# Optimization experiments

Hardware: AMD Instinct MI355X
Metric: run time of the kernel (lower is better)

## Reference

```python
import jax, jax.numpy as jnp
import numpy as np

BSZ, L, D_INNER, D_STATE = 2, 2048, 2048, 8
DT_RANK = D_INNER // 8  # 256


def setup_inputs() -> dict:
    key = jax.random.key(0)
    k0, k1, k2, k3 = jax.random.split(key, 4)
    x = jax.random.normal(k0, (BSZ, L, D_INNER), jnp.float32)
    # x_proj: Linear(d_inner -> dt_rank + 2*d_state), no bias
    W_xproj = jax.random.normal(k1, (DT_RANK + 2 * D_STATE, D_INNER), jnp.float32) * 0.02
    # dt_proj: Linear(dt_rank -> d_inner), uniform(-dt_rank^-0.5, +)
    std = DT_RANK ** -0.5
    W_dt = jax.random.uniform(k2, (D_INNER, DT_RANK), jnp.float32, -std, std)
    # dt bias init: inverse-softplus of dt ~ LogUniform(1e-3, 1e-1)
    dt = jnp.exp(jax.random.uniform(k3, (D_INNER,), jnp.float32)
                 * (jnp.log(0.1) - jnp.log(0.001)) + jnp.log(0.001))
    dt = jnp.clip(dt, 1e-4)
    b_dt = dt + jnp.log(-jnp.expm1(-dt))
    # A = repeat(arange(1, N+1), 'n -> d n'); A_log = log(A)
    A_log = jnp.log(jnp.broadcast_to(
        jnp.arange(1, D_STATE + 1, dtype=jnp.float32), (D_INNER, D_STATE)))
    D_param = jnp.ones((D_INNER,), jnp.float32)
    return {"x": x, "W_xproj": W_xproj, "W_dt": W_dt, "b_dt": b_dt,
            "A_log": A_log, "D_param": D_param}


def reference(x, W_xproj, W_dt, b_dt, A_log, D_param):
    # x: (B, L, D)
    d_state = A_log.shape[1]
    dt_rank = W_dt.shape[1]
    x_dbl = jnp.einsum('bld,kd->blk', x, W_xproj)          # (B,L,dt_rank+2N)
    dt_r = x_dbl[..., :dt_rank]
    B_ssm = x_dbl[..., dt_rank:dt_rank + d_state]          # (B,L,N)
    C_ssm = x_dbl[..., dt_rank + d_state:]                 # (B,L,N)
    delta = jax.nn.softplus(jnp.einsum('blr,dr->bld', dt_r, W_dt) + b_dt)  # (B,L,D) > 0
    A = -jnp.exp(A_log)                                     # (D,N) < 0
    # Discretization: dA = exp(delta*A), dBu = delta*B*u
    dA = jnp.exp(delta[..., None] * A)                      # (B,L,D,N)
    dBu = (delta * x)[..., None] * B_ssm[:, :, None, :]     # (B,L,D,N)

    # Linear recurrence h_t = dA_t * h_{t-1} + dBu_t via associative scan over L
    def combine(c1, c2):
        a1, b1 = c1
        a2, b2 = c2
        return a1 * a2, a2 * b1 + b2

    _, h = jax.lax.associative_scan(combine, (dA, dBu), axis=1)  # (B,L,D,N)
    y = jnp.einsum('bldn,bln->bld', h, C_ssm) + x * D_param
    return y
```

## Files before the change

### kernel.cpp

```cpp
#include <hip/hip_runtime.h>
#include <math.h>

#define BSZ    2
#define LSEQ   2048
#define DI     2048
#define DSTATE 8
#define DTRANK 256
#define KXP    (DTRANK + 2 * DSTATE)
#define NPAD   288
#define NC     64
#define CL     (LSEQ / NC)
#define KSPLIT 8

#define NWXP (288u * 2048u)
#define NWX  (272u * 2048u)
#define NWDT (2048u * 256u)

typedef __attribute__((ext_vector_type(8))) short bf16x8;
typedef __attribute__((ext_vector_type(4))) float f32x4;

static __device__ __forceinline__ unsigned short f2bf(float f) {
    unsigned u = __float_as_uint(f);
    u += 0x7fff + ((u >> 16) & 1);
    return (unsigned short)(u >> 16);
}
static __device__ __forceinline__ float bf2f(unsigned short s) {
    return __uint_as_float((unsigned)s << 16);
}

static __device__ __forceinline__ float softplus_fast(float z) {
    const float e = __expf(-fabsf(z));
    return fmaxf(z, 0.0f) + __logf(1.0f + e);
}

__global__ __launch_bounds__(256) void convert_w(const float* __restrict__ Wx,
                                                 const float* __restrict__ Wdt,
                                                 unsigned short* __restrict__ Wxb,
                                                 unsigned short* __restrict__ Wdtb) {
    const unsigned tid = blockIdx.x * 256 + threadIdx.x;
    const unsigned i4 = tid * 4;
    float4 v;
    unsigned short* dst;
    unsigned j;
    if (i4 < NWXP) {
        j = i4;
        v = (j < NWX) ? *(const float4*)&Wx[j] : make_float4(0.f, 0.f, 0.f, 0.f);
        dst = Wxb;
    } else {
        j = i4 - NWXP;
        if (j >= NWDT) return;
        v = *(const float4*)&Wdt[j];
        dst = Wdtb;
    }
    ushort4 o;
    o.x = f2bf(v.x); o.y = f2bf(v.y); o.z = f2bf(v.z); o.w = f2bf(v.w);
    *(ushort4*)&dst[j] = o;
}

__global__ __launch_bounds__(256) void gemm1_mfma(const float* __restrict__ x,
                                                  const unsigned short* __restrict__ Wxb,
                                                  unsigned short* __restrict__ partb) {
    const int mt   = blockIdx.x;
    const int ks   = blockIdx.y;
    const int wave = threadIdx.x >> 6;
    const int lane = threadIdx.x & 63;
    const int quad = lane >> 4;
    const int r    = lane & 15;
    const int kq   = quad * 8;
    const int rh   = wave >> 1;
    const int nh   = wave & 1;
    const int mbase  = mt * 32 + rh * 16;
    const int nfrag0 = nh * 9;
    const size_t arow = (size_t)(mbase + r) * DI;
    const size_t brow = (size_t)r * DI;

    f32x4 acc[9];
#pragma unroll
    for (int n = 0; n < 9; n++) acc[n] = (f32x4)(0.0f);

    const int kbeg = ks * (DI / KSPLIT);
#pragma unroll 2
    for (int k0 = kbeg; k0 < kbeg + DI / KSPLIT; k0 += 32) {
        const float4 u0 = *(const float4*)&x[arow + k0 + kq];
        const float4 u1 = *(const float4*)&x[arow + k0 + kq + 4];
        bf16x8 a;
        a[0] = (short)f2bf(u0.x); a[1] = (short)f2bf(u0.y);
        a[2] = (short)f2bf(u0.z); a[3] = (short)f2bf(u0.w);
        a[4] = (short)f2bf(u1.x); a[5] = (short)f2bf(u1.y);
        a[6] = (short)f2bf(u1.z); a[7] = (short)f2bf(u1.w);
#pragma unroll
        for (int nf = 0; nf < 9; nf++) {
            const bf16x8 b = *(const bf16x8*)&Wxb[brow + (size_t)(nfrag0 + nf) * (16 * DI) + k0 + kq];
            acc[nf] = __builtin_amdgcn_mfma_f32_16x16x32_bf16(a, b, acc[nf], 0, 0, 0);
        }
    }

    unsigned short* p = partb + (size_t)ks * 4096 * NPAD;
    const int row0 = mbase + quad * 4;
#pragma unroll
    for (int nf = 0; nf < 9; nf++) {
        const int col = (nfrag0 + nf) * 16 + r;
#pragma unroll
        for (int i = 0; i < 4; i++)
            p[(size_t)(row0 + i) * NPAD + col] = f2bf(acc[nf][i]);
    }
}

__global__ __launch_bounds__(256) void reduce1(const unsigned short* __restrict__ partb,
                                               float* __restrict__ xdbl,
                                               unsigned short* __restrict__ dtr) {
    const int tid = blockIdx.x * 256 + threadIdx.x;
    const int row = tid / 72;
    const int c4  = (tid - row * 72) * 4;
    float4 s = make_float4(0.f, 0.f, 0.f, 0.f);
#pragma unroll
    for (int ks = 0; ks < KSPLIT; ks++) {
        const ushort4 v = *(const ushort4*)&partb[(size_t)ks * 4096 * NPAD + (size_t)row * NPAD + c4];
        s.x += bf2f(v.x); s.y += bf2f(v.y); s.z += bf2f(v.z); s.w += bf2f(v.w);
    }
    if (c4 < KXP) *(float4*)&xdbl[(size_t)row * KXP + c4] = s;
    if (c4 < DTRANK) {
        ushort4 o;
        o.x = f2bf(s.x); o.y = f2bf(s.y); o.z = f2bf(s.z); o.w = f2bf(s.w);
        *(ushort4*)&dtr[(size_t)row * DTRANK + c4] = o;
    }
}

#define G2RS 40
__global__ __launch_bounds__(256, 2) void gemm2_mfma(const unsigned short* __restrict__ dtr,
                                                     const unsigned short* __restrict__ Wdtb,
                                                     const float* __restrict__ bdt,
                                                     float* __restrict__ delta) {
    __shared__ __align__(16) unsigned short As[128 * G2RS];
    __shared__ __align__(16) unsigned short Bs[128 * G2RS];
    const int nt   = blockIdx.x;
    const int mt   = blockIdx.y;
    const int t    = threadIdx.x;
    const int wave = t >> 6;
    const int lane = t & 63;
    const int quad = lane >> 4;
    const int r    = lane & 15;
    const int m0 = mt * 128, n0 = nt * 128;
    const int mw = (wave >> 1) * 64, nw = (wave & 1) * 64;

    const int srow = t >> 1;
    const int sc   = (t & 1) * 16;

    f32x4 acc[4][4];
#pragma unroll
    for (int f = 0; f < 4; f++)
#pragma unroll
        for (int g = 0; g < 4; g++) acc[f][g] = (f32x4)(0.0f);

    for (int k0 = 0; k0 < DTRANK; k0 += 32) {
        const bf16x8 a0 = *(const bf16x8*)&dtr[(size_t)(m0 + srow) * DTRANK + k0 + sc];
        const bf16x8 a1 = *(const bf16x8*)&dtr[(size_t)(m0 + srow) * DTRANK + k0 + sc + 8];
        const bf16x8 b0 = *(const bf16x8*)&Wdtb[(size_t)(n0 + srow) * DTRANK + k0 + sc];
        const bf16x8 b1 = *(const bf16x8*)&Wdtb[(size_t)(n0 + srow) * DTRANK + k0 + sc + 8];
        __syncthreads();
        *(bf16x8*)&As[srow * G2RS + sc]     = a0;
        *(bf16x8*)&As[srow * G2RS + sc + 8] = a1;
        *(bf16x8*)&Bs[srow * G2RS + sc]     = b0;
        *(bf16x8*)&Bs[srow * G2RS + sc + 8] = b1;
        __syncthreads();

        bf16x8 a[4], b[4];
#pragma unroll
        for (int f = 0; f < 4; f++)
            a[f] = *(const bf16x8*)&As[(mw + f * 16 + r) * G2RS + quad * 8];
#pragma unroll
        for (int g = 0; g < 4; g++)
            b[g] = *(const bf16x8*)&Bs[(nw + g * 16 + r) * G2RS + quad * 8];
#pragma unroll
        for (int f = 0; f < 4; f++)
#pragma unroll
            for (int g = 0; g < 4; g++)
                acc[f][g] = __builtin_amdgcn_mfma_f32_16x16x32_bf16(a[f], b[g], acc[f][g], 0, 0, 0);
    }

#pragma unroll
    for (int f = 0; f < 4; f++) {
        const int row0 = m0 + mw + f * 16 + quad * 4;
#pragma unroll
        for (int g = 0; g < 4; g++) {
            const int col = n0 + nw + g * 16 + r;
            const float bv = bdt[col];
#pragma unroll
            for (int i = 0; i < 4; i++)
                delta[(size_t)(row0 + i) * DI + col] = softplus_fast(acc[f][g][i] + bv);
        }
    }
}

__global__ __launch_bounds__(256) void scan_pass1(const float* __restrict__ x,
                                                  const float* __restrict__ delta,
                                                  const float* __restrict__ xdbl,
                                                  const float* __restrict__ Alog,
                                                  float* __restrict__ Pb,
                                                  float* __restrict__ Hb) {
    __shared__ __align__(16) float Ls[CL * 8];
    const int bi   = blockIdx.x;
    const int b    = bi >> 9;
    const int c    = (bi >> 3) & 63;
    const int dblk = bi & 7;
    const int d    = dblk * 256 + threadIdx.x;
    const int l0   = c * CL;
    const size_t row0 = (size_t)b * LSEQ + l0;

    if (threadIdx.x < CL * 2) {
        const int l = threadIdx.x >> 1, part = (threadIdx.x & 1) * 4;
        const float4 v = *(const float4*)&xdbl[(row0 + l) * KXP + DTRANK + part];
        *(float4*)&Ls[l * 8 + part] = v;
    }

    float A[8], h[8], P[8];
#pragma unroll
    for (int n = 0; n < 8; n++) {
        A[n] = -__expf(Alog[d * 8 + n]);
        h[n] = 0.f;
        P[n] = 1.f;
    }
    __syncthreads();

#pragma unroll 4
    for (int l = 0; l < CL; l++) {
        const size_t row = row0 + l;
        const float dl = delta[row * DI + d];
        const float xv = x[row * DI + d];
        const float du = dl * xv;
#pragma unroll
        for (int n = 0; n < 8; n++) {
            const float dA = __expf(dl * A[n]);
            h[n] = dA * h[n] + du * Ls[l * 8 + n];
            P[n] *= dA;
        }
    }
    const size_t base = ((size_t)(b * NC + c) * DI + d) * 8;
    *(float4*)&Pb[base]     = make_float4(P[0], P[1], P[2], P[3]);
    *(float4*)&Pb[base + 4] = make_float4(P[4], P[5], P[6], P[7]);
    *(float4*)&Hb[base]     = make_float4(h[0], h[1], h[2], h[3]);
    *(float4*)&Hb[base + 4] = make_float4(h[4], h[5], h[6], h[7]);
}

__global__ __launch_bounds__(256) void scan_pass2(const float* __restrict__ Pb,
                                                  const float* __restrict__ Hb,
                                                  float* __restrict__ h0) {
    const int t   = blockIdx.x * 256 + threadIdx.x;
    const int b   = t >> 14;
    const int rem = t & 16383;
    float h = 0.f;
#pragma unroll 4
    for (int c = 0; c < NC; c++) {
        const size_t base = (size_t)(b * NC + c) * (DI * 8) + rem;
        h0[base] = h;
        h = Pb[base] * h + Hb[base];
    }
}

__global__ __launch_bounds__(256) void scan_pass3(const float* __restrict__ x,
                                                  const float* __restrict__ delta,
                                                  const float* __restrict__ xdbl,
                                                  const float* __restrict__ Alog,
                                                  const float* __restrict__ Dp,
                                                  const float* __restrict__ h0,
                                                  float* __restrict__ y) {
    __shared__ __align__(16) float Ls[CL * 16];
    const int bi   = blockIdx.x;
    const int b    = bi >> 9;
    const int c    = (bi >> 3) & 63;
    const int dblk = bi & 7;
    const int d    = dblk * 256 + threadIdx.x;
    const int l0   = c * CL;
    const size_t row0 = (size_t)b * LSEQ + l0;

    if (threadIdx.x < CL * 4) {
        const int l = threadIdx.x >> 2, part = (threadIdx.x & 3) * 4;
        const float4 v = *(const float4*)&xdbl[(row0 + l) * KXP + DTRANK + part];
        *(float4*)&Ls[l * 16 + part] = v;
    }

    float A[8], h[8];
    const size_t hbase = ((size_t)(b * NC + c) * DI + d) * 8;
    const float4 h0a = *(const float4*)&h0[hbase];
    const float4 h0b = *(const float4*)&h0[hbase + 4];
    h[0] = h0a.x; h[1] = h0a.y; h[2] = h0a.z; h[3] = h0a.w;
    h[4] = h0b.x; h[5] = h0b.y; h[6] = h0b.z; h[7] = h0b.w;
#pragma unroll
    for (int n = 0; n < 8; n++) A[n] = -__expf(Alog[d * 8 + n]);
    const float Dpar = Dp[d];
    __syncthreads();

#pragma unroll 4
    for (int l = 0; l < CL; l++) {
        const size_t row = row0 + l;
        const float dl = delta[row * DI + d];
        const float xv = x[row * DI + d];
        const float du = dl * xv;
        float yv = 0.f;
#pragma unroll
        for (int n = 0; n < 8; n++) {
            const float dA = __expf(dl * A[n]);
            h[n] = dA * h[n] + du * Ls[l * 16 + n];
            yv += h[n] * Ls[l * 16 + 8 + n];
        }
        yv += xv * Dpar;
        y[row * DI + d] = yv;
    }
}

extern "C" void kernel_launch(void* const* d_in, const int* in_sizes, int n_in,
                              void* d_out, int out_size, void* d_ws, size_t ws_size,
                              hipStream_t stream) {
    const float* x    = (const float*)d_in[0];
    const float* Wx   = (const float*)d_in[1];
    const float* Wdt  = (const float*)d_in[2];
    const float* bdt  = (const float*)d_in[3];
    const float* Alog = (const float*)d_in[4];
    const float* Dp   = (const float*)d_in[5];
    float* y = (float*)d_out;

    float* ws    = (float*)d_ws;
    unsigned short* partb = (unsigned short*)ws;
    float* delta = ws;
    float* xdbl  = ws + 8388608;
    float* Pb    = xdbl + 1114112;
    float* Hb    = Pb + 2097152;
    float* h0    = Hb + 2097152;
    unsigned short* Wxb  = (unsigned short*)(h0 + 2097152);
    unsigned short* Wdtb = Wxb + (size_t)NWXP;
    unsigned short* dtr  = Wdtb + (size_t)NWDT;

    dim3 blk(256);
    hipLaunchKernelGGL(convert_w, dim3((NWXP + NWDT) / 4 / 256), blk, 0, stream,
                       Wx, Wdt, Wxb, Wdtb);
    hipLaunchKernelGGL(gemm1_mfma, dim3(128, KSPLIT), blk, 0, stream, x, Wxb, partb);
    hipLaunchKernelGGL(reduce1, dim3(4096 * 72 / 256), blk, 0, stream, partb, xdbl, dtr);
    hipLaunchKernelGGL(gemm2_mfma, dim3(16, 32), blk, 0, stream, dtr, Wdtb, bdt, delta);
    hipLaunchKernelGGL(scan_pass1, dim3(BSZ * NC * 8), blk, 0, stream, x, delta, xdbl, Alog, Pb, Hb);
    hipLaunchKernelGGL(scan_pass2, dim3(128), blk, 0, stream, Pb, Hb, h0);
    hipLaunchKernelGGL(scan_pass3, dim3(BSZ * NC * 8), blk, 0, stream, x, delta, xdbl, Alog, Dp, h0, y);
}
```

Baseline: 205.7 us.

## Stage gemm1 tiles through LDS with 64-row blocks for operand reuse

Rewrites the x_proj GEMM so each block loads a 64x32 x tile and the full 288x32 weight tile into shared memory, with padded rows, before running MFMAs. Each wave now computes 2x9 fragments instead of 1x9, so every B fragment is reused across two M fragments and weight global traffic per output is halved. The grid drops from 128 to 64 M-tiles. The price is two barriers per K step with no double buffering, more LDS use that may lower occupancy, and half as many blocks.

```diff
diff --git a/kernel.cpp b/kernel.cpp
--- a/kernel.cpp
+++ b/kernel.cpp
@@ -11,6 +11,7 @@
 #define NC     64
 #define CL     (LSEQ / NC)
 #define KSPLIT 8
+#define KCHUNK (DI / KSPLIT)
 
 #define NWXP (288u * 2048u)
 #define NWX  (272u * 2048u)
@@ -57,52 +58,83 @@
     *(ushort4*)&dst[j] = o;
 }
 
+#define G1RS 40
 __global__ __launch_bounds__(256) void gemm1_mfma(const float* __restrict__ x,
                                                   const unsigned short* __restrict__ Wxb,
                                                   unsigned short* __restrict__ partb) {
+    __shared__ __align__(16) unsigned short As[64 * G1RS];
+    __shared__ __align__(16) unsigned short Bs[288 * G1RS];
     const int mt   = blockIdx.x;
     const int ks   = blockIdx.y;
-    const int wave = threadIdx.x >> 6;
-    const int lane = threadIdx.x & 63;
+    const int t    = threadIdx.x;
+    const int wave = t >> 6;
+    const int lane = t & 63;
     const int quad = lane >> 4;
     const int r    = lane & 15;
-    const int kq   = quad * 8;
     const int rh   = wave >> 1;
     const int nh   = wave & 1;
-    const int mbase  = mt * 32 + rh * 16;
-    const int nfrag0 = nh * 9;
-    const size_t arow = (size_t)(mbase + r) * DI;
-    const size_t brow = (size_t)r * DI;
-
-    f32x4 acc[9];
-#pragma unroll
-    for (int n = 0; n < 9; n++) acc[n] = (f32x4)(0.0f);
-
-    const int kbeg = ks * (DI / KSPLIT);
-#pragma unroll 2
-    for (int k0 = kbeg; k0 < kbeg + DI / KSPLIT; k0 += 32) {
-        const float4 u0 = *(const float4*)&x[arow + k0 + kq];
-        const float4 u1 = *(const float4*)&x[arow + k0 + kq + 4];
-        bf16x8 a;
-        a[0] = (short)f2bf(u0.x); a[1] = (short)f2bf(u0.y);
-        a[2] = (short)f2bf(u0.z); a[3] = (short)f2bf(u0.w);
-        a[4] = (short)f2bf(u1.x); a[5] = (short)f2bf(u1.y);
-        a[6] = (short)f2bf(u1.z); a[7] = (short)f2bf(u1.w);
+    const int m0   = mt * 64;
+
+    const int arow = t >> 2;
+    const int aoff = (t & 3) * 8;
+
+    f32x4 acc[2][9];
+#pragma unroll
+    for (int f = 0; f < 2; f++)
+#pragma unroll
+        for (int n = 0; n < 9; n++) acc[f][n] = (f32x4)(0.0f);
+
+    const int kbeg = ks * KCHUNK;
+    for (int k0 = kbeg; k0 < kbeg + KCHUNK; k0 += 32) {
+        const float4 a0 = *(const float4*)&x[(size_t)(m0 + arow) * DI + k0 + aoff];
+        const float4 a1 = *(const float4*)&x[(size_t)(m0 + arow) * DI + k0 + aoff + 4];
+        bf16x8 bstage[5];
+#pragma unroll
+        for (int j = 0; j < 5; j++) {
+            const int i = t + j * 256;
+            if (i < 1152)
+                bstage[j] = *(const bf16x8*)&Wxb[(size_t)(i >> 2) * DI + k0 + (i & 3) * 8];
+        }
+        __syncthreads();
+        bf16x8 av;
+        av[0] = (short)f2bf(a0.x); av[1] = (short)f2bf(a0.y);
+        av[2] = (short)f2bf(a0.z); av[3] = (short)f2bf(a0.w);
+        av[4] = (short)f2bf(a1.x); av[5] = (short)f2bf(a1.y);
+        av[6] = (short)f2bf(a1.z); av[7] = (short)f2bf(a1.w);
+        *(bf16x8*)&As[arow * G1RS + aoff] = av;
+#pragma unroll
+        for (int j = 0; j < 5; j++) {
+            const int i = t + j * 256;
+            if (i < 1152)
+                *(bf16x8*)&Bs[(i >> 2) * G1RS + (i & 3) * 8] = bstage[j];
+        }
+        __syncthreads();
+
+        bf16x8 af[2], bf[9];
+#pragma unroll
+        for (int f = 0; f < 2; f++)
+            af[f] = *(const bf16x8*)&As[(rh * 32 + f * 16 + r) * G1RS + quad * 8];
+#pragma unroll
+        for (int nf = 0; nf < 9; nf++)
+            bf[nf] = *(const bf16x8*)&Bs[(nh * 144 + nf * 16 + r) * G1RS + quad * 8];
+#pragma unroll
+        for (int f = 0; f < 2; f++)
+#pragma unroll
+            for (int nf = 0; nf < 9; nf++)
+                acc[f][nf] = __builtin_amdgcn_mfma_f32_16x16x32_bf16(af[f], bf[nf], acc[f][nf], 0, 0, 0);
+    }
+
+    unsigned short* p = partb + (size_t)ks * 4096 * NPAD;
+#pragma unroll
+    for (int f = 0; f < 2; f++) {
+        const int row0 = m0 + rh * 32 + f * 16 + quad * 4;
 #pragma unroll
         for (int nf = 0; nf < 9; nf++) {
-            const bf16x8 b = *(const bf16x8*)&Wxb[brow + (size_t)(nfrag0 + nf) * (16 * DI) + k0 + kq];
-            acc[nf] = __builtin_amdgcn_mfma_f32_16x16x32_bf16(a, b, acc[nf], 0, 0, 0);
-        }
-    }
-
-    unsigned short* p = partb + (size_t)ks * 4096 * NPAD;
-    const int row0 = mbase + quad * 4;
-#pragma unroll
-    for (int nf = 0; nf < 9; nf++) {
-        const int col = (nfrag0 + nf) * 16 + r;
-#pragma unroll
-        for (int i = 0; i < 4; i++)
-            p[(size_t)(row0 + i) * NPAD + col] = f2bf(acc[nf][i]);
+            const int col = nh * 144 + nf * 16 + r;
+#pragma unroll
+            for (int i = 0; i < 4; i++)
+                p[(size_t)(row0 + i) * NPAD + col] = f2bf(acc[f][nf][i]);
+        }
     }
 }
 
@@ -333,7 +365,7 @@
     dim3 blk(256);
     hipLaunchKernelGGL(convert_w, dim3((NWXP + NWDT) / 4 / 256), blk, 0, stream,
                        Wx, Wdt, Wxb, Wdtb);
-    hipLaunchKernelGGL(gemm1_mfma, dim3(128, KSPLIT), blk, 0, stream, x, Wxb, partb);
+    hipLaunchKernelGGL(gemm1_mfma, dim3(64, KSPLIT), blk, 0, stream, x, Wxb, partb);
     hipLaunchKernelGGL(reduce1, dim3(4096 * 72 / 256), blk, 0, stream, partb, xdbl, dtr);
     hipLaunchKernelGGL(gemm2_mfma, dim3(16, 32), blk, 0, stream, dtr, Wdtb, bdt, delta);
     hipLaunchKernelGGL(scan_pass1, dim3(BSZ * NC * 8), blk, 0, stream, x, delta, xdbl, Alog, Pb, Hb);
```

Measured after the change: 181.8 us. 1.13x faster.
